# Kernel tuning notes

Hardware: AMD Instinct MI355X
Metric: run time of the kernel (lower is better)

Reference implementation:

```python
import jax, jax.numpy as jnp
import numpy as np

B = 256   # batch == nodes (required by the module's mask broadcasting)
N = 256
F = 128   # in_features
H = 4     # num_heads
D = 8     # out_features (per-head dim)
E_RAND = 8192


def setup_inputs() -> dict:
    key = jax.random.key(0)
    ks = jax.random.split(key, 10)
    x = jax.random.normal(ks[0], (B, N, F), jnp.float32)
    # random edges + self-loops so every adjacency row is non-empty
    e = jax.random.randint(ks[1], (2, E_RAND), 0, B)
    diag = jnp.stack([jnp.arange(B), jnp.arange(B)])
    edge_index = jnp.concatenate([e, diag], axis=1)  # [2, 8448]
    s_in = 1.0 / np.sqrt(F)
    s_hd = 1.0 / np.sqrt(H * D)
    Wq = jax.random.normal(ks[2], (F, H * D), jnp.float32) * s_in
    Wk = jax.random.normal(ks[3], (F, H * D), jnp.float32) * s_in
    Wv = jax.random.normal(ks[4], (F, H * D), jnp.float32) * s_in
    Wo = jax.random.normal(ks[5], (H * D, D), jnp.float32) * s_hd
    bq = jax.random.normal(ks[6], (H * D,), jnp.float32) * s_in
    bk = jax.random.normal(ks[7], (H * D,), jnp.float32) * s_in
    bv = jax.random.normal(ks[8], (H * D,), jnp.float32) * s_in
    bo = jax.random.normal(ks[9], (D,), jnp.float32) * s_hd
    return dict(x=x, edge_index=edge_index, Wq=Wq, bq=bq, Wk=Wk, bk=bk,
                Wv=Wv, bv=bv, Wo=Wo, bo=bo)


def reference(x, edge_index, Wq, bq, Wk, bk, Wv, bv, Wo, bo):
    Bn, Nn, _ = x.shape
    q = (x @ Wq + bq).reshape(Bn, Nn, H, D)
    k = (x @ Wk + bk).reshape(Bn, Nn, H, D)
    v = (x @ Wv + bv).reshape(Bn, Nn, H, D)
    # [B, H, N, N]
    scores = jnp.einsum('bqhd,bkhd->bhqk', q, k) / jnp.sqrt(jnp.float32(D))
    # dense adjacency from sparse edge list, as in the original
    adj = jnp.zeros((Bn, Bn), x.dtype).at[edge_index[0], edge_index[1]].set(1.0)
    # mask [B,B] broadcasts over trailing (q,k) dims since N == B
    scores = jnp.where(adj == 0, -jnp.inf, scores)
    attn = jax.nn.softmax(scores, axis=-1)
    out = jnp.einsum('bhqk,bkhd->bqhd', attn, v).reshape(Bn, Nn, H * D)
    return out @ Wo + bo
```

## Files before the change

### kernel.cpp

```cpp
#include <hip/hip_runtime.h>

typedef unsigned int u32;
typedef __fp16 h2v __attribute__((ext_vector_type(2)));
typedef __fp16 h4 __attribute__((ext_vector_type(4)));
typedef float f32x16 __attribute__((ext_vector_type(16)));

#define NB 256
#define NNODE 256
#define FF 128
#define DD 8
#define HDIM 32

__device__ __forceinline__ float dot2(h2v a, h2v b, float c) {
  return __builtin_amdgcn_fdot2(a, b, c, false);
}
__device__ __forceinline__ h2v bch2(u32 u) { return __builtin_bit_cast(h2v, u); }
__device__ __forceinline__ h4 bch4(uint2 u) { return __builtin_bit_cast(h4, u); }
__device__ __forceinline__ u32 bcu(h2v v) { return __builtin_bit_cast(u32, v); }
__device__ __forceinline__ f32x16 fzero() {
  f32x16 z;
  #pragma unroll
  for (int r = 0; r < 16; ++r) z[r] = 0.f;
  return z;
}
__device__ __forceinline__ f32x16 mfma8(h4 a, h4 b, f32x16 c) {
  return __builtin_amdgcn_mfma_f32_32x32x8f16(a, b, c, 0, 0, 0);
}

__global__ __launch_bounds__(256) void prep_w_kernel(
    const float* __restrict__ Wq, const float* __restrict__ bq,
    const float* __restrict__ Wk, const float* __restrict__ bk,
    const float* __restrict__ Wv, const float* __restrict__ bv,
    const float* __restrict__ Wo,
    u32* __restrict__ mask, u32* __restrict__ WtH, float* __restrict__ bias,
    u32* __restrict__ woT2)
{
  int g = blockIdx.x * 256 + threadIdx.x;
  if (g < 96 * 64) {
    int c = g >> 6, f = (g & 63) * 2;
    const float* W = (c < 32) ? Wq : ((c < 64) ? Wk : Wv);
    int cc = c & 31;
    WtH[g] = bcu(__builtin_amdgcn_cvt_pkrtz(W[f*HDIM + cc], W[(f+1)*HDIM + cc]));
  }
  if (g < NNODE * 8) mask[g] = 0u;
  if (g < 96) {
    const float* bb = (g < 32) ? bq : ((g < 64) ? bk : bv);
    bias[g] = bb[g & 31];
  }
  if (g < 128) {
    int d = g >> 4, p = g & 15;
    woT2[g] = bcu(__builtin_amdgcn_cvt_pkrtz(Wo[(2*p)*DD + d], Wo[(2*p+1)*DD + d]));
  }
}

__global__ __launch_bounds__(256) void prep_e_kernel(
    const int* __restrict__ eidx, int E, u32* __restrict__ mask)
{
  int e = blockIdx.x * 256 + threadIdx.x;
  if (e < E) {
    int r = eidx[e], c = eidx[E + e];
    atomicOr(&mask[r*8 + (c >> 5)], 1u << (c & 31));
  }
}

__global__ __launch_bounds__(256, 2) void fused_kernel(
    const float* __restrict__ x, const u32* __restrict__ WtH,
    const float* __restrict__ bias, const u32* __restrict__ mask,
    const u32* __restrict__ woT2, const float* __restrict__ bo,
    float* __restrict__ out)
{
  __shared__ u32 wLds[96 * 66];
  __shared__ __fp16 kS[NNODE * 36];
  __shared__ __fp16 vt32[32 * 260];
  __shared__ __fp16 oS[128 * 36];
  __shared__ u32 woS[128];
  __shared__ float boS[8];

  int t = threadIdx.x, lane = t & 63, w = t >> 6;
  int l31 = lane & 31, hi = lane >> 5;
  int b = blockIdx.x >> 1, half = blockIdx.x & 1;

  for (int g = t; g < 96 * 64; g += 256)
    wLds[(g >> 6) * 66 + (g & 63)] = WtH[g];
  if (t < 128) woS[t] = woT2[t];
  if (t < 8) boS[t] = bo[t];

  f32x16 aq, ak0, av0, ak1, av1;
  #pragma unroll
  for (int r = 0; r < 16; ++r) aq[r] = bias[(r & 3) + 8*(r >> 2) + 4*hi];
  {
    float bk_ = bias[32 + l31], bv_ = bias[64 + l31];
    #pragma unroll
    for (int r = 0; r < 16; ++r) { ak0[r]=bk_; av0[r]=bv_; ak1[r]=bk_; av1[r]=bv_; }
  }

  int node = half*128 + w*32 + l31;
  uint4 m0 = *(const uint4*)(mask + node * 8);
  uint4 m1 = *(const uint4*)(mask + node * 8 + 4);
  u32 mw8[8] = { m0.x, m0.y, m0.z, m0.w, m1.x, m1.y, m1.z, m1.w };
  #pragma unroll
  for (int i = 0; i < 8; ++i) mw8[i] = hi ? (mw8[i] >> 4) : mw8[i];

  __syncthreads();

  const float* xr0 = x + ((size_t)b * NNODE + w*32 + l31) * FF + 4 * hi;
  const float* xr1 = xr0 + (size_t)128 * FF;
  #pragma unroll
  for (int ks = 0; ks < 16; ++ks) {
    float4 xf0 = *(const float4*)(xr0 + ks * 8);
    float4 xf1 = *(const float4*)(xr1 + ks * 8);
    h2v a0 = __builtin_amdgcn_cvt_pkrtz(xf0.x, xf0.y);
    h2v b0 = __builtin_amdgcn_cvt_pkrtz(xf0.z, xf0.w);
    h4 f0 = __builtin_shufflevector(a0, b0, 0, 1, 2, 3);
    h2v a1 = __builtin_amdgcn_cvt_pkrtz(xf1.x, xf1.y);
    h2v b1 = __builtin_amdgcn_cvt_pkrtz(xf1.z, xf1.w);
    h4 f1 = __builtin_shufflevector(a1, b1, 0, 1, 2, 3);
    h4 wk = bch4(*(const uint2*)&wLds[(32 + l31)*66 + ks*4 + 2*hi]);
    h4 wv = bch4(*(const uint2*)&wLds[(64 + l31)*66 + ks*4 + 2*hi]);
    h4 wq = bch4(*(const uint2*)&wLds[l31*66 + ks*4 + 2*hi]);
    ak0 = mfma8(f0, wk, ak0);
    ak1 = mfma8(f1, wk, ak1);
    av0 = mfma8(f0, wv, av0);
    av1 = mfma8(f1, wv, av1);
    aq  = mfma8(wq, half ? f1 : f0, aq);
  }
  #pragma unroll
  for (int r = 0; r < 16; ++r) {
    int rc = (r & 3) + 8*(r >> 2) + 4*hi;
    int n0 = w*32 + rc, n1 = n0 + 128;
    kS[n0 * 36 + l31] = (__fp16)ak0[r];
    kS[n1 * 36 + l31] = (__fp16)ak1[r];
    vt32[l31 * 260 + n0] = (__fp16)av0[r];
    vt32[l31 * 260 + n1] = (__fp16)av1[r];
  }
  h4 Qf[4];
  #pragma unroll
  for (int h = 0; h < 4; ++h) {
    h2v qa = __builtin_amdgcn_cvt_pkrtz(aq[4*h],     aq[4*h + 1]);
    h2v qb = __builtin_amdgcn_cvt_pkrtz(aq[4*h + 2], aq[4*h + 3]);
    Qf[h] = __builtin_shufflevector(qa, qb, 0, 1, 2, 3);
  }
  __syncthreads();

  const float sc2 = 0.51006977f;
  const h2v one2 = bch2(0x3C003C00u);
  f32x16 accO[4] = { fzero(), fzero(), fzero(), fzero() };
  float lp[4] = { 0.f, 0.f, 0.f, 0.f };
  #pragma unroll
  for (int kt = 0; kt < 8; ++kt) {
    u32 mwh = mw8[kt];
    float mbv[16];
    #pragma unroll
    for (int r = 0; r < 16; ++r) {
      int bp = (r & 3) + 8*(r >> 2);
      mbv[r] = ((mwh >> bp) & 1u) ? -8.0f : -1e30f;
    }
    u32 pw[4][8];
    #pragma unroll
    for (int h = 0; h < 4; ++h) {
      h4 Kf = bch4(*(const uint2*)&kS[(kt*32 + l31)*36 + 8*h + 4*hi]);
      f32x16 T = mfma8(Kf, Qf[h], fzero());
      #pragma unroll
      for (int j = 0; j < 8; ++j) {
        float p0 = __builtin_amdgcn_exp2f(__builtin_fmaf(T[2*j],   sc2, mbv[2*j]));
        float p1 = __builtin_amdgcn_exp2f(__builtin_fmaf(T[2*j+1], sc2, mbv[2*j+1]));
        pw[h][j] = bcu(__builtin_amdgcn_cvt_pkrtz(p0, p1));
        lp[h] = dot2(bch2(pw[h][j]), one2, lp[h]);
      }
    }
    __builtin_amdgcn_s_setprio(1);
    #pragma unroll
    for (int kk = 0; kk < 4; ++kk) {
      h4 va = bch4(*(const uint2*)&vt32[l31*260 + kt*32 + kk*8 + 4*hi]);
      #pragma unroll
      for (int h = 0; h < 4; ++h)
        accO[h] = mfma8(va, bch4(make_uint2(pw[h][2*kk], pw[h][2*kk+1])), accO[h]);
    }
    __builtin_amdgcn_s_setprio(0);
  }
  #pragma unroll
  for (int h = 0; h < 4; ++h) {
    float lq = lp[h] + __shfl_xor(lp[h], 32);
    float inv = 1.0f / lq;
    h2v o0 = __builtin_amdgcn_cvt_pkrtz(accO[h][4*h]*inv,   accO[h][4*h+1]*inv);
    h2v o1 = __builtin_amdgcn_cvt_pkrtz(accO[h][4*h+2]*inv, accO[h][4*h+3]*inv);
    *(uint2*)&oS[(w*32 + l31)*36 + 8*h + 4*hi] = make_uint2(bcu(o0), bcu(o1));
  }
  __syncthreads();

  int pr = t >> 1, d4 = (t & 1) * 4;
  float r4[4] = { boS[d4], boS[d4+1], boS[d4+2], boS[d4+3] };
  #pragma unroll
  for (int p = 0; p < 16; ++p) {
    h2v o2 = bch2(*(const u32*)&oS[pr*36 + 2*p]);
    #pragma unroll
    for (int d = 0; d < 4; ++d)
      r4[d] = dot2(o2, bch2(woS[(d4 + d)*16 + p]), r4[d]);
  }
  float4 o = { r4[0], r4[1], r4[2], r4[3] };
  *(float4*)(out + ((size_t)b * NNODE + half*128 + pr) * DD + d4) = o;
}

extern "C" void kernel_launch(void* const* d_in, const int* in_sizes, int n_in,
                              void* d_out, int out_size, void* d_ws, size_t ws_size,
                              hipStream_t stream)
{
  const float* x  = (const float*)d_in[0];
  const int*   ei = (const int*)d_in[1];
  const float* Wq = (const float*)d_in[2];
  const float* bq = (const float*)d_in[3];
  const float* Wk = (const float*)d_in[4];
  const float* bk = (const float*)d_in[5];
  const float* Wv = (const float*)d_in[6];
  const float* bv = (const float*)d_in[7];
  const float* Wo = (const float*)d_in[8];
  const float* bo = (const float*)d_in[9];
  int E = in_sizes[1] / 2;

  char* ws = (char*)d_ws;
  u32*   mask = (u32*)(ws + 0);
  u32*   WtH  = (u32*)(ws + 8192);
  float* bias = (float*)(ws + 32768);
  u32*   woT2 = (u32*)(ws + 33280);

  prep_w_kernel<<<24, 256, 0, stream>>>(Wq, bq, Wk, bk, Wv, bv, Wo,
                                        mask, WtH, bias, woT2);
  prep_e_kernel<<<(E + 255) / 256, 256, 0, stream>>>(ei, E, mask);
  fused_kernel<<<NB * 2, 256, 0, stream>>>(x, WtH, bias, mask, woT2, bo,
                                           (float*)d_out);
}
```

Measured before the change: 41.75 us.

## Merge prep kernels, memset mask, remap block order, prefetch x loads

Merges the weight-prep and edge-scatter kernels into a single launch and clears the mask with hipMemsetAsync, so the mask zeroing no longer has to sit in the same kernel as the atomicOr scatter. Remaps the fused kernel's block index so the two halves of each batch land in different grid halves. Software-prefetches the next x float4 chunk in the projection loop to hide global load latency. Launch count stays the same (memset plus two kernels) and the prefetch adds register pressure.

```diff
diff --git a/kernel.cpp b/kernel.cpp
--- a/kernel.cpp
+++ b/kernel.cpp
@@ -27,11 +27,11 @@
   return __builtin_amdgcn_mfma_f32_32x32x8f16(a, b, c, 0, 0, 0);
 }
 
-__global__ __launch_bounds__(256) void prep_w_kernel(
+__global__ __launch_bounds__(256) void prep_kernel(
     const float* __restrict__ Wq, const float* __restrict__ bq,
     const float* __restrict__ Wk, const float* __restrict__ bk,
     const float* __restrict__ Wv, const float* __restrict__ bv,
-    const float* __restrict__ Wo,
+    const float* __restrict__ Wo, const int* __restrict__ eidx, int E,
     u32* __restrict__ mask, u32* __restrict__ WtH, float* __restrict__ bias,
     u32* __restrict__ woT2)
 {
@@ -42,7 +42,6 @@
     int cc = c & 31;
     WtH[g] = bcu(__builtin_amdgcn_cvt_pkrtz(W[f*HDIM + cc], W[(f+1)*HDIM + cc]));
   }
-  if (g < NNODE * 8) mask[g] = 0u;
   if (g < 96) {
     const float* bb = (g < 32) ? bq : ((g < 64) ? bk : bv);
     bias[g] = bb[g & 31];
@@ -51,14 +50,8 @@
     int d = g >> 4, p = g & 15;
     woT2[g] = bcu(__builtin_amdgcn_cvt_pkrtz(Wo[(2*p)*DD + d], Wo[(2*p+1)*DD + d]));
   }
-}
-
-__global__ __launch_bounds__(256) void prep_e_kernel(
-    const int* __restrict__ eidx, int E, u32* __restrict__ mask)
-{
-  int e = blockIdx.x * 256 + threadIdx.x;
-  if (e < E) {
-    int r = eidx[e], c = eidx[E + e];
+  if (g < E) {
+    int r = eidx[g], c = eidx[E + g];
     atomicOr(&mask[r*8 + (c >> 5)], 1u << (c & 31));
   }
 }
@@ -78,7 +71,7 @@
 
   int t = threadIdx.x, lane = t & 63, w = t >> 6;
   int l31 = lane & 31, hi = lane >> 5;
-  int b = blockIdx.x >> 1, half = blockIdx.x & 1;
+  int b = blockIdx.x & 255, half = blockIdx.x >> 8;
 
   for (int g = t; g < 96 * 64; g += 256)
     wLds[(g >> 6) * 66 + (g & 63)] = WtH[g];
@@ -105,15 +98,20 @@
 
   const float* xr0 = x + ((size_t)b * NNODE + w*32 + l31) * FF + 4 * hi;
   const float* xr1 = xr0 + (size_t)128 * FF;
+  float4 xc0 = *(const float4*)(xr0);
+  float4 xc1 = *(const float4*)(xr1);
   #pragma unroll
   for (int ks = 0; ks < 16; ++ks) {
-    float4 xf0 = *(const float4*)(xr0 + ks * 8);
-    float4 xf1 = *(const float4*)(xr1 + ks * 8);
-    h2v a0 = __builtin_amdgcn_cvt_pkrtz(xf0.x, xf0.y);
-    h2v b0 = __builtin_amdgcn_cvt_pkrtz(xf0.z, xf0.w);
+    float4 xn0, xn1;
+    if (ks < 15) {
+      xn0 = *(const float4*)(xr0 + (ks + 1) * 8);
+      xn1 = *(const float4*)(xr1 + (ks + 1) * 8);
+    }
+    h2v a0 = __builtin_amdgcn_cvt_pkrtz(xc0.x, xc0.y);
+    h2v b0 = __builtin_amdgcn_cvt_pkrtz(xc0.z, xc0.w);
     h4 f0 = __builtin_shufflevector(a0, b0, 0, 1, 2, 3);
-    h2v a1 = __builtin_amdgcn_cvt_pkrtz(xf1.x, xf1.y);
-    h2v b1 = __builtin_amdgcn_cvt_pkrtz(xf1.z, xf1.w);
+    h2v a1 = __builtin_amdgcn_cvt_pkrtz(xc1.x, xc1.y);
+    h2v b1 = __builtin_amdgcn_cvt_pkrtz(xc1.z, xc1.w);
     h4 f1 = __builtin_shufflevector(a1, b1, 0, 1, 2, 3);
     h4 wk = bch4(*(const uint2*)&wLds[(32 + l31)*66 + ks*4 + 2*hi]);
     h4 wv = bch4(*(const uint2*)&wLds[(64 + l31)*66 + ks*4 + 2*hi]);
@@ -123,6 +121,7 @@
     av0 = mfma8(f0, wv, av0);
     av1 = mfma8(f1, wv, av1);
     aq  = mfma8(wq, half ? f1 : f0, aq);
+    xc0 = xn0; xc1 = xn1;
   }
   #pragma unroll
   for (int r = 0; r < 16; ++r) {
@@ -223,9 +222,10 @@
   float* bias = (float*)(ws + 32768);
   u32*   woT2 = (u32*)(ws + 33280);
 
-  prep_w_kernel<<<24, 256, 0, stream>>>(Wq, bq, Wk, bk, Wv, bv, Wo,
-                                        mask, WtH, bias, woT2);
-  prep_e_kernel<<<(E + 255) / 256, 256, 0, stream>>>(ei, E, mask);
+  hipMemsetAsync(mask, 0, NNODE * 8 * sizeof(u32), stream);
+  int prep_work = (96*64 > E) ? 96*64 : E;
+  prep_kernel<<<(prep_work + 255)/256, 256, 0, stream>>>(
+      Wq, bq, Wk, bk, Wv, bv, Wo, ei, E, mask, WtH, bias, woT2);
   fused_kernel<<<NB * 2, 256, 0, stream>>>(x, WtH, bias, mask, woT2, bo,
                                            (float*)d_out);
 }
```

After: 39.50 us. 1.06x faster.
